# Performance work log

Hardware: AMD Instinct MI355X
Metric: run time of the kernel (lower is better)

## Reference

```python
import jax, jax.numpy as jnp
import numpy as np

B, IN, H = 8192, 1024, 1024


def setup_inputs() -> dict:
    key = jax.random.key(0)
    ks = jax.random.split(key, 16)
    s_in = 1.0 / np.sqrt(IN)
    s_h = 1.0 / np.sqrt(H)
    d = {}
    d['x'] = jax.random.normal(ks[0], (B, IN), jnp.float32)
    d['h'] = jax.random.normal(ks[1], (B, H), jnp.float32)
    d['c_prev'] = jax.random.normal(ks[2], (B, H), jnp.float32)
    d['W_fx'] = jax.random.normal(ks[3], (H, IN), jnp.float32) * s_in
    d['b_f'] = jax.random.normal(ks[4], (H,), jnp.float32) * s_in
    d['W_fh'] = jax.random.normal(ks[5], (H, H), jnp.float32) * s_h
    d['W_ix'] = jax.random.normal(ks[6], (H, IN), jnp.float32) * s_in
    d['b_i'] = jax.random.normal(ks[7], (H,), jnp.float32) * s_in
    d['W_ih'] = jax.random.normal(ks[8], (H, H), jnp.float32) * s_h
    d['W_gx'] = jax.random.normal(ks[9], (H, IN), jnp.float32) * s_in
    d['b_g'] = jax.random.normal(ks[10], (H,), jnp.float32) * s_in
    d['W_gh'] = jax.random.normal(ks[11], (H, H), jnp.float32) * s_h
    d['W_ox'] = jax.random.normal(ks[12], (H, IN), jnp.float32) * s_in
    d['b_o'] = jax.random.normal(ks[13], (H,), jnp.float32) * s_in
    d['W_oh'] = jax.random.normal(ks[14], (H, H), jnp.float32) * s_h
    return d


def reference(x, h, c_prev, W_fx, b_f, W_fh, W_ix, b_i, W_ih,
              W_gx, b_g, W_gh, W_ox, b_o, W_oh):
    # Concatenate the four x-projections and four h-projections into two
    # fused GEMMs (same math as the 8 separate nn.Linear calls).
    Wx = jnp.concatenate([W_ix, W_fx, W_gx, W_ox], axis=0)  # [4H, IN]
    Wh = jnp.concatenate([W_ih, W_fh, W_gh, W_oh], axis=0)  # [4H, H]
    bx = jnp.concatenate([b_i, b_f, b_g, b_o], axis=0)       # [4H]
    z = x @ Wx.T + h @ Wh.T + bx                              # [B, 4H]
    zi, zf, zg, zo = jnp.split(z, 4, axis=-1)
    i = jax.nn.sigmoid(zi)
    f = jax.nn.sigmoid(zf)
    g = jnp.tanh(zg)
    o = jax.nn.sigmoid(zo)
    c_next = f * c_prev + i * g
    h_next = o * jnp.tanh(c_next)
    return (h_next, c_next)
```

## Files before the change

kernel.cpp:

```cpp
#include <hip/hip_runtime.h>
#include <stdint.h>

typedef unsigned short ushort_t;
typedef __attribute__((ext_vector_type(8))) short short8;
typedef __attribute__((ext_vector_type(4))) float floatx4;

#define B_   8192
#define IN_  1024
#define H_   1024

#define XB_ELEMS   (B_ * IN_)
#define WB_ELEMS   (H_ * IN_)
#define WS_XB   0
#define WS_HB   XB_ELEMS
#define WS_WB   (2 * XB_ELEMS)

__device__ __forceinline__ ushort_t f2bf(float f) {
    union { float f; uint32_t i; } v; v.f = f;
    uint32_t r = (v.i + 0x7fffu + ((v.i >> 16) & 1u)) >> 16;
    return (ushort_t)r;
}
__device__ __forceinline__ float sigmoid_(float x) {
    return 1.0f / (1.0f + __expf(-x));
}
__device__ __forceinline__ float tanh_(float x) {
    float xc = fminf(fmaxf(x, -20.f), 20.f);
    float e = __expf(2.f * xc);
    return (e - 1.f) / (e + 1.f);
}

__device__ __forceinline__ void gll16(const ushort_t* gsrc, ushort_t* ldst) {
    __builtin_amdgcn_global_load_lds(
        (const __attribute__((address_space(1))) void*)gsrc,
        (__attribute__((address_space(3))) void*)ldst,
        16, 0, 0);
}

__global__ __launch_bounds__(256) void cvt_kernel(
    const float* __restrict__ X,   const float* __restrict__ Hin,
    const float* __restrict__ Wix, const float* __restrict__ Wfx,
    const float* __restrict__ Wgx, const float* __restrict__ Wox,
    const float* __restrict__ Wih, const float* __restrict__ Wfh,
    const float* __restrict__ Wgh, const float* __restrict__ Woh,
    ushort_t* __restrict__ ws)
{
    const int c = blockIdx.x * 256 + threadIdx.x;
    const float* src;
    ushort_t* dst;
    int off;
    if (c < 2097152) {
        const int t = c >> 20;
        src = t ? Hin : X;
        dst = ws + (t ? WS_HB : WS_XB);
        off = (c & 1048575) * 8;
    } else {
        const int cc = c - 2097152;
        const int s = cc >> 17;
        const float* w =
            s == 0 ? Wix : s == 1 ? Wfx : s == 2 ? Wgx : s == 3 ? Wox :
            s == 4 ? Wih : s == 5 ? Wfh : s == 6 ? Wgh : Woh;
        src = w;
        dst = ws + WS_WB + s * WB_ELEMS;
        off = (cc & 131071) * 8;
    }
    float4 f0 = *(const float4*)(src + off);
    float4 f1 = *(const float4*)(src + off + 4);
    short8 o;
    o[0] = (short)f2bf(f0.x); o[1] = (short)f2bf(f0.y);
    o[2] = (short)f2bf(f0.z); o[3] = (short)f2bf(f0.w);
    o[4] = (short)f2bf(f1.x); o[5] = (short)f2bf(f1.y);
    o[6] = (short)f2bf(f1.z); o[7] = (short)f2bf(f1.w);
    *(short8*)(dst + off) = o;
}


#define BAR()  __builtin_amdgcn_s_barrier()
#define LGKM0() do{ asm volatile("s_waitcnt lgkmcnt(0)" ::: "memory"); \
                    __builtin_amdgcn_sched_barrier(0); }while(0)
#define VMC(N) asm volatile("s_waitcnt vmcnt(" #N ")" ::: "memory")

#define STAGE_A(TS, KH, DS) do{ \
    const ushort_t* _s = (((TS) < 16) ? Xb : Hb) + (((TS) & 15) * 64 + (KH) * 32); \
    ushort_t* _d = lds + ((DS) * 32768 + (KH) * 8192); \
    gll16(_s + aoff0,          _d + t * 8); \
    gll16(_s + aoff0 + 131072, _d + 4096 + t * 8); \
  }while(0)

#define STAGE_B(TS, KH, DS) do{ \
    const ushort_t* _s = Wb + ((((TS) < 16) ? 0 : 4 * WB_ELEMS) + (((TS) & 15) * 64 + (KH) * 32)); \
    ushort_t* _d = lds + ((DS) * 32768 + 16384 + (KH) * 8192); \
    gll16(_s + boff0,         _d + t * 8); \
    gll16(_s + boff0 + 32768, _d + 4096 + t * 8); \
  }while(0)

#define RD_A(S, KH, RF) (*(const short8*)(lds + ((S) * 32768 + (KH) * 8192) + a_rd + (RF) * 512))
#define RD_B(S, KH, CT) (*(const short8*)(lds + ((S) * 32768 + 16384 + (KH) * 8192) + b_rd + (CT) * 512))

#define MFMA16(RFB) do{ \
    __builtin_amdgcn_s_setprio(1); \
    _Pragma("unroll") \
    for (int _rf = 0; _rf < 4; ++_rf) \
      _Pragma("unroll") \
      for (int _ct = 0; _ct < 4; ++_ct) \
        acc[(RFB) + _rf][_ct] = __builtin_amdgcn_mfma_f32_16x16x32_bf16( \
            af[_rf], bf[_ct], acc[(RFB) + _rf][_ct], 0, 0, 0); \
    __builtin_amdgcn_s_setprio(0); \
  }while(0)

#define KTILE(T, S, ST01, ST23, VMSTMT) do{ \
     \
    _Pragma("unroll") for (int _r = 0; _r < 4; ++_r) af[_r] = RD_A(S, 0, _r); \
    _Pragma("unroll") for (int _c = 0; _c < 4; ++_c) bf[_c] = RD_B(S, 0, _c); \
    if (ST01) STAGE_A((T) + 1, 1, (S) ^ 1); \
    BAR(); LGKM0(); MFMA16(0); BAR(); \
     \
    _Pragma("unroll") for (int _r = 0; _r < 4; ++_r) af[_r] = RD_A(S, 0, 4 + _r); \
    if (ST01) STAGE_B((T) + 1, 1, (S) ^ 1); \
    BAR(); LGKM0(); MFMA16(4); BAR(); \
     \
    _Pragma("unroll") for (int _r = 0; _r < 4; ++_r) af[_r] = RD_A(S, 1, _r); \
    _Pragma("unroll") for (int _c = 0; _c < 4; ++_c) bf[_c] = RD_B(S, 1, _c); \
    if (ST23) STAGE_A((T) + 2, 0, S); \
    BAR(); LGKM0(); MFMA16(0); BAR(); \
     \
    _Pragma("unroll") for (int _r = 0; _r < 4; ++_r) af[_r] = RD_A(S, 1, 4 + _r); \
    if (ST23) STAGE_B((T) + 2, 0, S); \
    BAR(); LGKM0(); MFMA16(4); VMSTMT; BAR(); \
  }while(0)

__global__ __launch_bounds__(512, 2) void lstm_cell_kernel(
    const ushort_t* __restrict__ Xb,  const ushort_t* __restrict__ Hb,
    const ushort_t* __restrict__ Wb,
    const float* __restrict__ Cprev,
    const float* __restrict__ Bi, const float* __restrict__ Bf,
    const float* __restrict__ Bg, const float* __restrict__ Bo,
    float* __restrict__ Out)
{
    __shared__ __align__(16) ushort_t lds[65536];

    const int t   = threadIdx.x;
    const int bm0 = blockIdx.y * 256;
    const int j0  = blockIdx.x * 64;

    const int r0 = t >> 2;
    const int c0 = (t & 3) ^ ((t >> 3) & 3);
    const int aoff0 = (bm0 + r0) * 1024 + c0 * 8;
    const int g0  = (r0 >> 4) & 3;
    const int jv0 = j0 + ((r0 >> 6) << 4) + (r0 & 15);
    const int boff0 = g0 * WB_ELEMS + jv0 * 1024 + c0 * 8;

    const int lane = t & 63;
    const int wid  = t >> 6;
    const int wr = wid >> 2, wc = wid & 3;
    const int lr = lane & 15, lk = lane >> 4;
    const int xk = lk ^ ((lr >> 1) & 3);
    const int a_rd = (wr * 512 + lr * 4 + xk) * 8;
    const int b_rd = (wc * 256 + lr * 4 + xk) * 8;

    short8 af[4], bf[4];
    floatx4 acc[8][4] = {};

    STAGE_A(0, 0, 0); STAGE_B(0, 0, 0);
    STAGE_A(0, 1, 0); STAGE_B(0, 1, 0);
    STAGE_A(1, 0, 1); STAGE_B(1, 0, 1);
    VMC(4);
    BAR();

    for (int T = 0; T < 30; T += 2) {
        KTILE(T,     0, 1, 1, VMC(4));
        KTILE(T + 1, 1, 1, 1, VMC(4));
    }
    KTILE(30, 0, 1, 0, VMC(0));
    KTILE(31, 1, 0, 0, (void)0);

    const int j = j0 + wc * 16 + lr;
    const float bi = Bi[j], bff = Bf[j], bg = Bg[j], bo = Bo[j];

    #pragma unroll
    for (int rf = 0; rf < 8; ++rf) {
        #pragma unroll
        for (int reg = 0; reg < 4; ++reg) {
            const int m = bm0 + wr * 128 + rf * 16 + lk * 4 + reg;
            const float zi = acc[rf][0][reg] + bi;
            const float zf = acc[rf][1][reg] + bff;
            const float zg = acc[rf][2][reg] + bg;
            const float zo = acc[rf][3][reg] + bo;
            const float ig = sigmoid_(zi);
            const float fg = sigmoid_(zf);
            const float gg = tanh_(zg);
            const float og = sigmoid_(zo);
            const float cp = Cprev[(size_t)m * H_ + j];
            const float cn = fg * cp + ig * gg;
            const float hn = og * tanh_(cn);
            Out[(size_t)m * H_ + j] = hn;
            Out[(size_t)B_ * H_ + (size_t)m * H_ + j] = cn;
        }
    }
}

extern "C" void kernel_launch(void* const* d_in, const int* in_sizes, int n_in,
                              void* d_out, int out_size, void* d_ws, size_t ws_size,
                              hipStream_t stream)
{
    (void)in_sizes; (void)n_in; (void)out_size; (void)ws_size;
    const float* X   = (const float*)d_in[0];
    const float* Hin = (const float*)d_in[1];
    const float* Cp  = (const float*)d_in[2];
    const float* Wfx = (const float*)d_in[3];
    const float* Bf  = (const float*)d_in[4];
    const float* Wfh = (const float*)d_in[5];
    const float* Wix = (const float*)d_in[6];
    const float* Bi  = (const float*)d_in[7];
    const float* Wih = (const float*)d_in[8];
    const float* Wgx = (const float*)d_in[9];
    const float* Bg  = (const float*)d_in[10];
    const float* Wgh = (const float*)d_in[11];
    const float* Wox = (const float*)d_in[12];
    const float* Bo  = (const float*)d_in[13];
    const float* Woh = (const float*)d_in[14];
    float* Out = (float*)d_out;
    ushort_t* ws  = (ushort_t*)d_ws;

    cvt_kernel<<<dim3(12288), dim3(256), 0, stream>>>(
        X, Hin, Wix, Wfx, Wgx, Wox, Wih, Wfh, Wgh, Woh, ws);

    dim3 grid(H_ / 64, B_ / 256);
    lstm_cell_kernel<<<grid, dim3(512), 0, stream>>>(
        ws + WS_XB, ws + WS_HB, ws + WS_WB,
        Cp, Bi, Bf, Bg, Bo, Out);
}
```

Measured before the change: 314.1 us.

## Fuse fp32-to-bf16 conversion of X and H into the GEMM A-operand load path

Drops the separate conversion pass over the activations X and H. The GEMM kernel now loads their fp32 values into registers, converts them to bf16, and writes them to LDS with a reworked software-pipelined K loop. Weights are still converted in a smaller pre-pass. This removes a full write and re-read of 32 MB of bf16 activations, but it reads 2x the activation bytes per tile, because each A tile is reloaded by 16 column blocks. It also adds register pressure and VALU conversion work inside the main loop.

```diff
diff --git a/kernel.cpp b/kernel.cpp
--- a/kernel.cpp
+++ b/kernel.cpp
@@ -9,11 +9,7 @@
 #define IN_  1024
 #define H_   1024
 
-#define XB_ELEMS   (B_ * IN_)
 #define WB_ELEMS   (H_ * IN_)
-#define WS_XB   0
-#define WS_HB   XB_ELEMS
-#define WS_WB   (2 * XB_ELEMS)
 
 __device__ __forceinline__ ushort_t f2bf(float f) {
     union { float f; uint32_t i; } v; v.f = f;
@@ -37,7 +33,6 @@
 }
 
 __global__ __launch_bounds__(256) void cvt_kernel(
-    const float* __restrict__ X,   const float* __restrict__ Hin,
     const float* __restrict__ Wix, const float* __restrict__ Wfx,
     const float* __restrict__ Wgx, const float* __restrict__ Wox,
     const float* __restrict__ Wih, const float* __restrict__ Wfh,
@@ -45,26 +40,14 @@
     ushort_t* __restrict__ ws)
 {
     const int c = blockIdx.x * 256 + threadIdx.x;
-    const float* src;
-    ushort_t* dst;
-    int off;
-    if (c < 2097152) {
-        const int t = c >> 20;
-        src = t ? Hin : X;
-        dst = ws + (t ? WS_HB : WS_XB);
-        off = (c & 1048575) * 8;
-    } else {
-        const int cc = c - 2097152;
-        const int s = cc >> 17;
-        const float* w =
-            s == 0 ? Wix : s == 1 ? Wfx : s == 2 ? Wgx : s == 3 ? Wox :
-            s == 4 ? Wih : s == 5 ? Wfh : s == 6 ? Wgh : Woh;
-        src = w;
-        dst = ws + WS_WB + s * WB_ELEMS;
-        off = (cc & 131071) * 8;
-    }
-    float4 f0 = *(const float4*)(src + off);
-    float4 f1 = *(const float4*)(src + off + 4);
+    const int s = c >> 17;
+    const float* w =
+        s == 0 ? Wix : s == 1 ? Wfx : s == 2 ? Wgx : s == 3 ? Wox :
+        s == 4 ? Wih : s == 5 ? Wfh : s == 6 ? Wgh : Woh;
+    const int off = (c & 131071) * 8;
+    ushort_t* dst = ws + s * WB_ELEMS;
+    float4 f0 = *(const float4*)(w + off);
+    float4 f1 = *(const float4*)(w + off + 4);
     short8 o;
     o[0] = (short)f2bf(f0.x); o[1] = (short)f2bf(f0.y);
     o[2] = (short)f2bf(f0.z); o[3] = (short)f2bf(f0.w);
@@ -75,16 +58,31 @@
 
 
 #define BAR()  __builtin_amdgcn_s_barrier()
-#define LGKM0() do{ asm volatile("s_waitcnt lgkmcnt(0)" ::: "memory"); \
-                    __builtin_amdgcn_sched_barrier(0); }while(0)
-#define VMC(N) asm volatile("s_waitcnt vmcnt(" #N ")" ::: "memory")
-
-#define STAGE_A(TS, KH, DS) do{ \
-    const ushort_t* _s = (((TS) < 16) ? Xb : Hb) + (((TS) & 15) * 64 + (KH) * 32); \
-    ushort_t* _d = lds + ((DS) * 32768 + (KH) * 8192); \
-    gll16(_s + aoff0,          _d + t * 8); \
-    gll16(_s + aoff0 + 131072, _d + 4096 + t * 8); \
-  }while(0)
+#define WAIT_VM(N) do{ asm volatile("s_waitcnt vmcnt(" #N ")" ::: "memory"); \
+                       __builtin_amdgcn_sched_barrier(0); }while(0)
+#define LGKM0() asm volatile("s_waitcnt lgkmcnt(0)" ::: "memory")
+
+#define ISSUE_A(R0, R1, R2, R3, T2, KH) do{ \
+    const float* _a0 = (((T2) < 16) ? Xf : Hf) + (((T2) & 15) * 64 + (KH) * 32) + aIdx0; \
+    R0 = *(const floatx4*)(_a0); \
+    R1 = *(const floatx4*)(_a0 + 4); \
+    R2 = *(const floatx4*)(_a0 + 131072); \
+    R3 = *(const floatx4*)(_a0 + 131076); \
+}while(0)
+
+#define CVT_WRITE(R0, R1, R2, R3, DS, KH) do{ \
+    short8 _o0, _o1; \
+    _o0[0]=(short)f2bf(R0.x); _o0[1]=(short)f2bf(R0.y); \
+    _o0[2]=(short)f2bf(R0.z); _o0[3]=(short)f2bf(R0.w); \
+    _o0[4]=(short)f2bf(R1.x); _o0[5]=(short)f2bf(R1.y); \
+    _o0[6]=(short)f2bf(R1.z); _o0[7]=(short)f2bf(R1.w); \
+    _o1[0]=(short)f2bf(R2.x); _o1[1]=(short)f2bf(R2.y); \
+    _o1[2]=(short)f2bf(R2.z); _o1[3]=(short)f2bf(R2.w); \
+    _o1[4]=(short)f2bf(R3.x); _o1[5]=(short)f2bf(R3.y); \
+    _o1[6]=(short)f2bf(R3.z); _o1[7]=(short)f2bf(R3.w); \
+    *(short8*)(lds + (DS)*32768 + (KH)*8192 + t*8)        = _o0; \
+    *(short8*)(lds + (DS)*32768 + (KH)*8192 + 4096 + t*8) = _o1; \
+}while(0)
 
 #define STAGE_B(TS, KH, DS) do{ \
     const ushort_t* _s = Wb + ((((TS) < 16) ? 0 : 4 * WB_ELEMS) + (((TS) & 15) * 64 + (KH) * 32)); \
@@ -103,33 +101,39 @@
       _Pragma("unroll") \
       for (int _ct = 0; _ct < 4; ++_ct) \
         acc[(RFB) + _rf][_ct] = __builtin_amdgcn_mfma_f32_16x16x32_bf16( \
-            af[_rf], bf[_ct], acc[(RFB) + _rf][_ct], 0, 0, 0); \
+            af[_rf], bfr[_ct], acc[(RFB) + _rf][_ct], 0, 0, 0); \
     __builtin_amdgcn_s_setprio(0); \
   }while(0)
 
-#define KTILE(T, S, ST01, ST23, VMSTMT) do{ \
-     \
-    _Pragma("unroll") for (int _r = 0; _r < 4; ++_r) af[_r] = RD_A(S, 0, _r); \
-    _Pragma("unroll") for (int _c = 0; _c < 4; ++_c) bf[_c] = RD_B(S, 0, _c); \
-    if (ST01) STAGE_A((T) + 1, 1, (S) ^ 1); \
-    BAR(); LGKM0(); MFMA16(0); BAR(); \
-     \
-    _Pragma("unroll") for (int _r = 0; _r < 4; ++_r) af[_r] = RD_A(S, 0, 4 + _r); \
-    if (ST01) STAGE_B((T) + 1, 1, (S) ^ 1); \
-    BAR(); LGKM0(); MFMA16(4); BAR(); \
-     \
-    _Pragma("unroll") for (int _r = 0; _r < 4; ++_r) af[_r] = RD_A(S, 1, _r); \
-    _Pragma("unroll") for (int _c = 0; _c < 4; ++_c) bf[_c] = RD_B(S, 1, _c); \
-    if (ST23) STAGE_A((T) + 2, 0, S); \
-    BAR(); LGKM0(); MFMA16(0); BAR(); \
-     \
-    _Pragma("unroll") for (int _r = 0; _r < 4; ++_r) af[_r] = RD_A(S, 1, 4 + _r); \
-    if (ST23) STAGE_B((T) + 2, 0, S); \
-    BAR(); LGKM0(); MFMA16(4); VMSTMT; BAR(); \
-  }while(0)
+#define KTILE_STEADY(T, S) do{ \
+     \
+    af[0]=RD_A(S,0,0); bfr[0]=RD_B(S,0,0); af[1]=RD_A(S,0,1); bfr[1]=RD_B(S,0,1); \
+    af[2]=RD_A(S,0,2); bfr[2]=RD_B(S,0,2); af[3]=RD_A(S,0,3); bfr[3]=RD_B(S,0,3); \
+    ISSUE_A(a00,a01,a02,a03, (T)+2, 0); \
+    BAR(); MFMA16(0); \
+    WAIT_VM(6); \
+    CVT_WRITE(a10,a11,a12,a13, (S)^1, 1);    \
+    LGKM0(); BAR(); \
+     \
+    af[0]=RD_A(S,0,4); af[1]=RD_A(S,0,5); af[2]=RD_A(S,0,6); af[3]=RD_A(S,0,7); \
+    STAGE_B((T)+1, 1, (S)^1); \
+    BAR(); MFMA16(4); BAR(); \
+     \
+    af[0]=RD_A(S,1,0); bfr[0]=RD_B(S,1,0); af[1]=RD_A(S,1,1); bfr[1]=RD_B(S,1,1); \
+    af[2]=RD_A(S,1,2); bfr[2]=RD_B(S,1,2); af[3]=RD_A(S,1,3); bfr[3]=RD_B(S,1,3); \
+    ISSUE_A(a10,a11,a12,a13, (T)+2, 1); \
+    BAR(); MFMA16(0); \
+    WAIT_VM(6); \
+    CVT_WRITE(a00,a01,a02,a03, S, 0);        \
+    LGKM0(); BAR(); \
+     \
+    af[0]=RD_A(S,1,4); af[1]=RD_A(S,1,5); af[2]=RD_A(S,1,6); af[3]=RD_A(S,1,7); \
+    STAGE_B((T)+2, 0, S); \
+    BAR(); MFMA16(4); BAR(); \
+}while(0)
 
 __global__ __launch_bounds__(512, 2) void lstm_cell_kernel(
-    const ushort_t* __restrict__ Xb,  const ushort_t* __restrict__ Hb,
+    const float* __restrict__ Xf,  const float* __restrict__ Hf,
     const ushort_t* __restrict__ Wb,
     const float* __restrict__ Cprev,
     const float* __restrict__ Bi, const float* __restrict__ Bf,
@@ -144,7 +148,7 @@
 
     const int r0 = t >> 2;
     const int c0 = (t & 3) ^ ((t >> 3) & 3);
-    const int aoff0 = (bm0 + r0) * 1024 + c0 * 8;
+    const int aIdx0 = (bm0 + r0) * 1024 + c0 * 8;
     const int g0  = (r0 >> 4) & 3;
     const int jv0 = j0 + ((r0 >> 6) << 4) + (r0 & 15);
     const int boff0 = g0 * WB_ELEMS + jv0 * 1024 + c0 * 8;
@@ -157,21 +161,59 @@
     const int a_rd = (wr * 512 + lr * 4 + xk) * 8;
     const int b_rd = (wc * 256 + lr * 4 + xk) * 8;
 
-    short8 af[4], bf[4];
+    short8 af[4], bfr[4];
+    floatx4 a00, a01, a02, a03, a10, a11, a12, a13;
+    floatx4 p10, p11, p12, p13, p20, p21, p22, p23;
     floatx4 acc[8][4] = {};
 
-    STAGE_A(0, 0, 0); STAGE_B(0, 0, 0);
-    STAGE_A(0, 1, 0); STAGE_B(0, 1, 0);
-    STAGE_A(1, 0, 1); STAGE_B(1, 0, 1);
-    VMC(4);
+    ISSUE_A(a00,a01,a02,a03, 0, 0);
+    ISSUE_A(p10,p11,p12,p13, 0, 1);
+    ISSUE_A(p20,p21,p22,p23, 1, 0);
+    STAGE_B(0, 0, 0); STAGE_B(0, 1, 0);
+    ISSUE_A(a10,a11,a12,a13, 1, 1);
+    STAGE_B(1, 0, 1);
+    WAIT_VM(0);
+    CVT_WRITE(a00,a01,a02,a03, 0, 0);
+    CVT_WRITE(p10,p11,p12,p13, 0, 1);
+    CVT_WRITE(p20,p21,p22,p23, 1, 0);
+    LGKM0();
     BAR();
 
     for (int T = 0; T < 30; T += 2) {
-        KTILE(T,     0, 1, 1, VMC(4));
-        KTILE(T + 1, 1, 1, 1, VMC(4));
-    }
-    KTILE(30, 0, 1, 0, VMC(0));
-    KTILE(31, 1, 0, 0, (void)0);
+        KTILE_STEADY(T,     0);
+        KTILE_STEADY(T + 1, 1);
+    }
+
+    {
+        af[0]=RD_A(0,0,0); bfr[0]=RD_B(0,0,0); af[1]=RD_A(0,0,1); bfr[1]=RD_B(0,0,1);
+        af[2]=RD_A(0,0,2); bfr[2]=RD_B(0,0,2); af[3]=RD_A(0,0,3); bfr[3]=RD_B(0,0,3);
+        BAR(); MFMA16(0);
+        WAIT_VM(2);
+        CVT_WRITE(a10,a11,a12,a13, 1, 1);
+        LGKM0(); BAR();
+        af[0]=RD_A(0,0,4); af[1]=RD_A(0,0,5); af[2]=RD_A(0,0,6); af[3]=RD_A(0,0,7);
+        STAGE_B(31, 1, 1);
+        BAR(); MFMA16(4); BAR();
+        af[0]=RD_A(0,1,0); bfr[0]=RD_B(0,1,0); af[1]=RD_A(0,1,1); bfr[1]=RD_B(0,1,1);
+        af[2]=RD_A(0,1,2); bfr[2]=RD_B(0,1,2); af[3]=RD_A(0,1,3); bfr[3]=RD_B(0,1,3);
+        BAR(); MFMA16(0); BAR();
+        af[0]=RD_A(0,1,4); af[1]=RD_A(0,1,5); af[2]=RD_A(0,1,6); af[3]=RD_A(0,1,7);
+        BAR(); MFMA16(4);
+        WAIT_VM(0);
+        BAR();
+    }
+    {
+        af[0]=RD_A(1,0,0); bfr[0]=RD_B(1,0,0); af[1]=RD_A(1,0,1); bfr[1]=RD_B(1,0,1);
+        af[2]=RD_A(1,0,2); bfr[2]=RD_B(1,0,2); af[3]=RD_A(1,0,3); bfr[3]=RD_B(1,0,3);
+        BAR(); MFMA16(0); BAR();
+        af[0]=RD_A(1,0,4); af[1]=RD_A(1,0,5); af[2]=RD_A(1,0,6); af[3]=RD_A(1,0,7);
+        BAR(); MFMA16(4); BAR();
+        af[0]=RD_A(1,1,0); bfr[0]=RD_B(1,1,0); af[1]=RD_A(1,1,1); bfr[1]=RD_B(1,1,1);
+        af[2]=RD_A(1,1,2); bfr[2]=RD_B(1,1,2); af[3]=RD_A(1,1,3); bfr[3]=RD_B(1,1,3);
+        BAR(); MFMA16(0); BAR();
+        af[0]=RD_A(1,1,4); af[1]=RD_A(1,1,5); af[2]=RD_A(1,1,6); af[3]=RD_A(1,1,7);
+        BAR(); MFMA16(4); BAR();
+    }
 
     const int j = j0 + wc * 16 + lr;
     const float bi = Bi[j], bff = Bf[j], bg = Bg[j], bo = Bo[j];
@@ -221,11 +263,10 @@
     float* Out = (float*)d_out;
     ushort_t* ws  = (ushort_t*)d_ws;
 
-    cvt_kernel<<<dim3(12288), dim3(256), 0, stream>>>(
-        X, Hin, Wix, Wfx, Wgx, Wox, Wih, Wfh, Wgh, Woh, ws);
+    cvt_kernel<<<dim3(4096), dim3(256), 0, stream>>>(
+        Wix, Wfx, Wgx, Wox, Wih, Wfh, Wgh, Woh, ws);
 
     dim3 grid(H_ / 64, B_ / 256);
     lstm_cell_kernel<<<grid, dim3(512), 0, stream>>>(
-        ws + WS_XB, ws + WS_HB, ws + WS_WB,
-        Cp, Bi, Bf, Bg, Bo, Out);
-}
+        X, Hin, ws, Cp, Bi, Bf, Bg, Bo, Out);
+}
```

Result: slower. 342.9 us (+9.2%).

## Double-buffer MFMA register fragments and overlap LDS reads with MFMA

Applied to the files above, without the earlier changes.

Splits the A/B register fragments into two sets so the LDS reads for the next quarter-tile are issued while the current quarter's MFMAs run. The first fragments of the next K-tile are prefetched at the end of each tile. This drops the explicit lgkmcnt(0) waits with their scheduling barriers and halves the barriers per quarter. The global-load wait points move from vmcnt(4) to vmcnt(2). The aim is to hide LDS latency behind matrix-core work, at the cost of higher register pressure and tighter barrier/ordering correctness.

```diff
diff --git a/kernel.cpp b/kernel.cpp
--- a/kernel.cpp
+++ b/kernel.cpp
@@ -75,9 +75,7 @@
 
 
 #define BAR()  __builtin_amdgcn_s_barrier()
-#define LGKM0() do{ asm volatile("s_waitcnt lgkmcnt(0)" ::: "memory"); \
-                    __builtin_amdgcn_sched_barrier(0); }while(0)
-#define VMC(N) asm volatile("s_waitcnt vmcnt(" #N ")" ::: "memory")
+#define WAIT_VM(N) asm volatile("s_waitcnt vmcnt(" #N ")" ::: "memory")
 
 #define STAGE_A(TS, KH, DS) do{ \
     const ushort_t* _s = (((TS) < 16) ? Xb : Hb) + (((TS) & 15) * 64 + (KH) * 32); \
@@ -96,37 +94,47 @@
 #define RD_A(S, KH, RF) (*(const short8*)(lds + ((S) * 32768 + (KH) * 8192) + a_rd + (RF) * 512))
 #define RD_B(S, KH, CT) (*(const short8*)(lds + ((S) * 32768 + 16384 + (KH) * 8192) + b_rd + (CT) * 512))
 
-#define MFMA16(RFB) do{ \
+#define MFMA16(AF, BF, RFB) do{ \
     __builtin_amdgcn_s_setprio(1); \
     _Pragma("unroll") \
     for (int _rf = 0; _rf < 4; ++_rf) \
       _Pragma("unroll") \
       for (int _ct = 0; _ct < 4; ++_ct) \
         acc[(RFB) + _rf][_ct] = __builtin_amdgcn_mfma_f32_16x16x32_bf16( \
-            af[_rf], bf[_ct], acc[(RFB) + _rf][_ct], 0, 0, 0); \
+            AF[_rf], BF[_ct], acc[(RFB) + _rf][_ct], 0, 0, 0); \
     __builtin_amdgcn_s_setprio(0); \
   }while(0)
 
-#define KTILE(T, S, ST01, ST23, VMSTMT) do{ \
-     \
-    _Pragma("unroll") for (int _r = 0; _r < 4; ++_r) af[_r] = RD_A(S, 0, _r); \
-    _Pragma("unroll") for (int _c = 0; _c < 4; ++_c) bf[_c] = RD_B(S, 0, _c); \
+#define KTILE(T, S, ST01, ST23, PRE, VMQ) do{ \
+     \
+    BAR(); \
     if (ST01) STAGE_A((T) + 1, 1, (S) ^ 1); \
-    BAR(); LGKM0(); MFMA16(0); BAR(); \
-     \
-    _Pragma("unroll") for (int _r = 0; _r < 4; ++_r) af[_r] = RD_A(S, 0, 4 + _r); \
+    afB[0]=RD_A(S,0,4); afB[1]=RD_A(S,0,5); afB[2]=RD_A(S,0,6); afB[3]=RD_A(S,0,7); \
+    bB[0]=RD_B(S,1,0);  bB[1]=RD_B(S,1,1); \
+    MFMA16(afA, bA, 0); \
+     \
+    BAR(); \
     if (ST01) STAGE_B((T) + 1, 1, (S) ^ 1); \
-    BAR(); LGKM0(); MFMA16(4); BAR(); \
-     \
-    _Pragma("unroll") for (int _r = 0; _r < 4; ++_r) af[_r] = RD_A(S, 1, _r); \
-    _Pragma("unroll") for (int _c = 0; _c < 4; ++_c) bf[_c] = RD_B(S, 1, _c); \
+    afA[0]=RD_A(S,1,0); afA[1]=RD_A(S,1,1); afA[2]=RD_A(S,1,2); afA[3]=RD_A(S,1,3); \
+    bB[2]=RD_B(S,1,2);  bB[3]=RD_B(S,1,3); \
+    MFMA16(afB, bA, 4); \
+     \
+    BAR(); \
     if (ST23) STAGE_A((T) + 2, 0, S); \
-    BAR(); LGKM0(); MFMA16(0); BAR(); \
-     \
-    _Pragma("unroll") for (int _r = 0; _r < 4; ++_r) af[_r] = RD_A(S, 1, 4 + _r); \
+    afB[0]=RD_A(S,1,4); afB[1]=RD_A(S,1,5); afB[2]=RD_A(S,1,6); afB[3]=RD_A(S,1,7); \
+    MFMA16(afA, bB, 0); \
+    VMQ; \
+     \
+    BAR(); \
     if (ST23) STAGE_B((T) + 2, 0, S); \
-    BAR(); LGKM0(); MFMA16(4); VMSTMT; BAR(); \
-  }while(0)
+    if (PRE) { \
+      afA[0]=RD_A((S)^1,0,0); bA[0]=RD_B((S)^1,0,0); \
+      afA[1]=RD_A((S)^1,0,1); bA[1]=RD_B((S)^1,0,1); \
+      afA[2]=RD_A((S)^1,0,2); bA[2]=RD_B((S)^1,0,2); \
+      afA[3]=RD_A((S)^1,0,3); bA[3]=RD_B((S)^1,0,3); \
+    } \
+    MFMA16(afB, bB, 4); \
+}while(0)
 
 __global__ __launch_bounds__(512, 2) void lstm_cell_kernel(
     const ushort_t* __restrict__ Xb,  const ushort_t* __restrict__ Hb,
@@ -157,21 +165,25 @@
     const int a_rd = (wr * 512 + lr * 4 + xk) * 8;
     const int b_rd = (wc * 256 + lr * 4 + xk) * 8;
 
-    short8 af[4], bf[4];
+    short8 afA[4], afB[4], bA[4], bB[4];
     floatx4 acc[8][4] = {};
 
     STAGE_A(0, 0, 0); STAGE_B(0, 0, 0);
     STAGE_A(0, 1, 0); STAGE_B(0, 1, 0);
     STAGE_A(1, 0, 1); STAGE_B(1, 0, 1);
-    VMC(4);
+    WAIT_VM(0);
     BAR();
+    afA[0]=RD_A(0,0,0); bA[0]=RD_B(0,0,0);
+    afA[1]=RD_A(0,0,1); bA[1]=RD_B(0,0,1);
+    afA[2]=RD_A(0,0,2); bA[2]=RD_B(0,0,2);
+    afA[3]=RD_A(0,0,3); bA[3]=RD_B(0,0,3);
 
     for (int T = 0; T < 30; T += 2) {
-        KTILE(T,     0, 1, 1, VMC(4));
-        KTILE(T + 1, 1, 1, 1, VMC(4));
+        KTILE(T,     0, 1, 1, 1, WAIT_VM(2));
+        KTILE(T + 1, 1, 1, 1, 1, WAIT_VM(2));
     }
-    KTILE(30, 0, 1, 0, VMC(0));
-    KTILE(31, 1, 0, 0, (void)0);
+    KTILE(30, 0, 1, 0, 1, WAIT_VM(0));
+    KTILE(31, 1, 0, 0, 0, (void)0);
 
     const int j = j0 + wc * 16 + lr;
     const float bi = Bi[j], bff = Bf[j], bg = Bg[j], bo = Bo[j];
```

Result: no change. 319.5 us (+1.7%).
